# Optimization experiments

Measured on AMD Instinct MI355X. Metric: run time of the kernel, lower is better.

Reference implementation:

```python
import jax, jax.numpy as jnp
import numpy as np

H = 32        # num_attention_heads
KVH = 8       # num_key_value_heads
D = 64        # attention_head_size
WIN = 256     # attention_window_size (left/right)
ROPE_BASE = 10000.0


def setup_inputs() -> dict:
    key = jax.random.key(0)
    k1, k2, k3 = jax.random.split(key, 3)
    B, S = 2, 2048
    return {
        "query_states": jax.random.normal(k1, (B, S, H * D), dtype=jnp.float32),
        "key_states": jax.random.normal(k2, (B, S, KVH * D), dtype=jnp.float32),
        "value_states": jax.random.normal(k3, (B, S, KVH * D), dtype=jnp.float32),
    }


def _rope_cos_sin(seq_len, dtype):
    inv_freq = 1.0 / (ROPE_BASE ** (jnp.arange(0, D, 2, dtype=jnp.float32) / D))  # [D/2]
    pos = jnp.arange(seq_len, dtype=jnp.float32)
    freqs = pos[:, None] * inv_freq[None, :]          # [S, D/2]
    emb = jnp.concatenate([freqs, freqs], axis=-1)    # [S, D]
    return jnp.cos(emb).astype(dtype), jnp.sin(emb).astype(dtype)


def _rotate_half(x):
    x1, x2 = x[..., : D // 2], x[..., D // 2 :]
    return jnp.concatenate([-x2, x1], axis=-1)


def reference(query_states, key_states, value_states):
    B, S, _ = query_states.shape
    n_rep = H // KVH

    q = query_states.reshape(B, S, H, D).transpose(0, 2, 1, 3)        # [B,H,S,D]
    k = key_states.reshape(B, S, KVH, D).transpose(0, 2, 1, 3)        # [B,KVH,S,D]
    v = value_states.reshape(B, S, KVH, D).transpose(0, 2, 1, 3)

    # repeat_kv: [B,KVH,S,D] -> [B,H,S,D]
    k = jnp.repeat(k, n_rep, axis=1)
    v = jnp.repeat(v, n_rep, axis=1)

    cos, sin = _rope_cos_sin(S, q.dtype)   # [S,D]
    cos = cos[None, None]                  # [1,1,S,D]
    sin = sin[None, None]
    q = q * cos + _rotate_half(q) * sin
    k = k * cos + _rotate_half(k) * sin

    scale = 1.0 / jnp.sqrt(jnp.asarray(D, dtype=q.dtype))
    scores = jnp.einsum("bhqd,bhkd->bhqk", q, k) * scale              # [B,H,S,S]

    i = jnp.arange(S)[:, None]
    j = jnp.arange(S)[None, :]
    allowed = (j >= i - WIN) & (j <= i)                               # [S,S]
    scores = jnp.where(allowed[None, None], scores, jnp.finfo(scores.dtype).min)

    probs = jax.nn.softmax(scores, axis=-1)
    out = jnp.einsum("bhqk,bhkd->bhqd", probs, v)                     # [B,H,S,D]
    return out.transpose(0, 2, 1, 3).reshape(B, S, H * D)
```

## Files before the change

### kernel.cpp

```cpp
#include <hip/hip_runtime.h>
#include <math.h>

#define NH   32
#define NKVH 8
#define HD   64
#define WIN  256
#define BB   2
#define SS   2048

typedef short short8 __attribute__((ext_vector_type(8)));
typedef float f32x4  __attribute__((ext_vector_type(4)));

__device__ __forceinline__ ushort f2bf(float x) {
    union { float f; unsigned u; } v; v.f = x;
    unsigned u = v.u + 0x7FFF + ((v.u >> 16) & 1);
    return (ushort)(u >> 16);
}

__device__ __forceinline__ int cvtpk_bf16(float lo, float hi) {
    int r;
    asm("v_cvt_pk_bf16_f32 %0, %1, %2" : "=v"(r) : "v"(lo), "v"(hi));
    return r;
}

__device__ __forceinline__ int swz(int L) { return L ^ (((L >> 7) & 7) << 4); }

__device__ __forceinline__ void stage16(const void* g, void* l) {
    __builtin_amdgcn_global_load_lds(
        (const __attribute__((address_space(1))) unsigned int*)g,
        (__attribute__((address_space(3))) unsigned int*)l, 16, 0, 0);
}

__global__ __launch_bounds__(256) void prep_kv(const float* __restrict__ K,
                                               const float* __restrict__ V,
                                               ushort* __restrict__ Kr,
                                               ushort* __restrict__ Vt) {
    __shared__ __align__(16) ushort ldsK[2048];
    __shared__ __align__(16) ushort ldsV[2048];
    const int bidx = blockIdx.x;
    const int sblk = bidx & 63;
    const int s0   = sblk * 32;
    const int kvh  = (bidx >> 6) & 7;
    const int b    = bidx >> 9;
    const int tid  = threadIdx.x;

    {
        const int key = tid >> 3, dg = tid & 7;
        const int s   = s0 + key;
        const float* krow = K + (size_t)(b * SS + s) * (NKVH * HD) + kvh * HD + dg * 8;
        float x[8];
        *(float4*)(x)     = *(const float4*)(krow);
        *(float4*)(x + 4) = *(const float4*)(krow + 4);
        float inv = __powf(10000.f, -(float)((dg & 3) * 8) * (1.f / 32.f));
        const float ratio = 0.74989420933f;
        ushort out[8];
#pragma unroll
        for (int j = 0; j < 8; ++j) {
            float partner = __shfl(x[j], (tid & 63) ^ 4, 64);
            float sn, cs;
            __sincosf((float)s * inv, &sn, &cs);
            out[j] = f2bf(x[j] * cs + ((dg < 4) ? -partner : partner) * sn);
            inv *= ratio;
        }
        *(short8*)((char*)ldsK + swz(key * 128 + dg * 16)) = *(short8*)out;
    }
    {
        const int kp = tid & 15, dq = tid >> 4;
        const float* v0 = V + (size_t)(b * SS + s0 + 2 * kp) * (NKVH * HD) + kvh * HD + dq * 4;
        float4 a = *(const float4*)v0;
        float4 c = *(const float4*)(v0 + NKVH * HD);
#pragma unroll
        for (int j = 0; j < 4; ++j) {
            int d = dq * 4 + j;
            unsigned w = (unsigned)f2bf(((const float*)&a)[j])
                       | ((unsigned)f2bf(((const float*)&c)[j]) << 16);
            *(unsigned*)((char*)ldsV + swz(d * 64 + kp * 4)) = w;
        }
    }
    __syncthreads();
    char* kc = (char*)(Kr + (size_t)(b * NKVH + kvh) * SS * HD) + (size_t)sblk * 4096;
    char* vc = (char*)(Vt + (size_t)(b * NKVH + kvh) * HD * SS) + (size_t)sblk * 4096;
    *(short8*)(kc + tid * 16) = *(short8*)((char*)ldsK + tid * 16);
    *(short8*)(vc + tid * 16) = *(short8*)((char*)ldsV + tid * 16);
}

__global__ __launch_bounds__(256, 4) void attn_mfma(const float* __restrict__ Q,
                                                    const ushort* __restrict__ Kr,
                                                    const ushort* __restrict__ Vt,
                                                    float* __restrict__ O) {
    __shared__ __align__(16) ushort ldsK[2][2048];
    __shared__ __align__(16) ushort ldsV[2][2048];
    const int wv = threadIdx.x >> 6, lane = threadIdx.x & 63;
    const int lo16 = lane & 15, quad = lane >> 4;
    const int bidx = (blockIdx.x & 7) * 128 + (blockIdx.x >> 3);
    const int qblk = bidx & 63;
    const int kvh  = (bidx >> 6) & 7;
    const int b    = bidx >> 9;
    const int h    = kvh * 4 + wv;
    const int q0   = qblk * 32;

    float invf[8];
#pragma unroll
    for (int j = 0; j < 8; ++j)
        invf[j] = __powf(10000.f, -(float)(quad * 8 + j) * (1.f / 32.f));

    short8 aq[2][2];
#pragma unroll
    for (int t = 0; t < 2; ++t) {
        int qi = q0 + t * 16 + lo16;
        const float* qrow = Q + (size_t)(b * SS + qi) * (NH * HD) + h * HD;
        float lo[8], hi[8];
        *(float4*)(lo)     = *(const float4*)(qrow + quad * 8);
        *(float4*)(lo + 4) = *(const float4*)(qrow + quad * 8 + 4);
        *(float4*)(hi)     = *(const float4*)(qrow + 32 + quad * 8);
        *(float4*)(hi + 4) = *(const float4*)(qrow + 32 + quad * 8 + 4);
#pragma unroll
        for (int j = 0; j < 8; ++j) {
            float sn, cs;
            __sincosf((float)qi * invf[j], &sn, &cs);
            aq[t][0][j] = (short)f2bf((lo[j] * cs - hi[j] * sn) * 0.125f);
            aq[t][1][j] = (short)f2bf((hi[j] * cs + lo[j] * sn) * 0.125f);
        }
    }

    const char* kbase = (const char*)(Kr + (size_t)(b * NKVH + kvh) * SS * HD);
    const char* vbase = (const char*)(Vt + (size_t)(b * NKVH + kvh) * HD * SS);

    f32x4 acc[2][4];
#pragma unroll
    for (int t = 0; t < 2; ++t)
#pragma unroll
        for (int i = 0; i < 4; ++i) acc[t][i] = (f32x4){0.f, 0.f, 0.f, 0.f};
    float psum[2] = {0.f, 0.f};

    const int idxAB = (lo16 + ((quad & 1) << 5)) << 2;
    const int idxCD = idxAB + 64;
    const bool hiq  = quad >= 2;

    int klo = q0 - WIN; if (klo < 0) klo = 0;
    const int c0  = klo >> 5;
    const int cnt = (q0 >> 5) - c0 + 1;

    {
        const char* kc = kbase + (size_t)c0 * 4096 + wv * 1024 + lane * 16;
        const char* vc = vbase + (size_t)c0 * 4096 + wv * 1024 + lane * 16;
        stage16(kc, (char*)&ldsK[0][0] + wv * 1024);
        stage16(vc, (char*)&ldsV[0][0] + wv * 1024);
    }
    __syncthreads();

    int nb = 0;
    for (int it = 0; it < cnt; ++it, nb ^= 1) {
        const int kb = klo + it * 32;
        if (it + 1 < cnt) {
            const char* kc = kbase + (size_t)(c0 + it + 1) * 4096 + wv * 1024 + lane * 16;
            const char* vc = vbase + (size_t)(c0 + it + 1) * 4096 + wv * 1024 + lane * 16;
            stage16(kc, (char*)&ldsK[nb ^ 1][0] + wv * 1024);
            stage16(vc, (char*)&ldsV[nb ^ 1][0] + wv * 1024);
        }

        const char* kl = (const char*)&ldsK[nb][0];
        short8 k0 = *(const short8*)(kl + swz(lo16 * 128 + quad * 16));
        short8 k1 = *(const short8*)(kl + swz(lo16 * 128 + 64 + quad * 16));
        short8 k2 = *(const short8*)(kl + swz((lo16 + 16) * 128 + quad * 16));
        short8 k3 = *(const short8*)(kl + swz((lo16 + 16) * 128 + 64 + quad * 16));

        const f32x4 z = {0.f, 0.f, 0.f, 0.f};
        __builtin_amdgcn_s_setprio(1);
        f32x4 s00 = __builtin_amdgcn_mfma_f32_16x16x32_bf16(k0, aq[0][0], z,   0, 0, 0);
        s00       = __builtin_amdgcn_mfma_f32_16x16x32_bf16(k1, aq[0][1], s00, 0, 0, 0);
        f32x4 s01 = __builtin_amdgcn_mfma_f32_16x16x32_bf16(k2, aq[0][0], z,   0, 0, 0);
        s01       = __builtin_amdgcn_mfma_f32_16x16x32_bf16(k3, aq[0][1], s01, 0, 0, 0);
        f32x4 s10 = __builtin_amdgcn_mfma_f32_16x16x32_bf16(k0, aq[1][0], z,   0, 0, 0);
        s10       = __builtin_amdgcn_mfma_f32_16x16x32_bf16(k1, aq[1][1], s10, 0, 0, 0);
        f32x4 s11 = __builtin_amdgcn_mfma_f32_16x16x32_bf16(k2, aq[1][0], z,   0, 0, 0);
        s11       = __builtin_amdgcn_mfma_f32_16x16x32_bf16(k3, aq[1][1], s11, 0, 0, 0);
        __builtin_amdgcn_s_setprio(0);

        short8 ap[2];
#pragma unroll
        for (int t = 0; t < 2; ++t) {
            const f32x4 sa = t ? s10 : s00;
            const f32x4 sb = t ? s11 : s01;
            const int qtmin = q0 + t * 16;
            const int myq   = qtmin + lo16;
            float p[8];
            if ((kb + 31 > qtmin) || (kb < qtmin + 15 - WIN)) {
#pragma unroll
                for (int r = 0; r < 4; ++r) {
                    int key0 = kb + quad * 4 + r;
                    int key1 = key0 + 16;
                    p[r]     = (key0 <= myq && key0 >= myq - WIN) ? __expf(sa[r]) : 0.f;
                    p[4 + r] = (key1 <= myq && key1 >= myq - WIN) ? __expf(sb[r]) : 0.f;
                }
            } else {
#pragma unroll
                for (int r = 0; r < 4; ++r) { p[r] = __expf(sa[r]); p[4 + r] = __expf(sb[r]); }
            }
            psum[t] += ((p[0] + p[1]) + (p[2] + p[3])) + ((p[4] + p[5]) + (p[6] + p[7]));

            int w0 = cvtpk_bf16(p[0], p[1]);
            int w1 = cvtpk_bf16(p[2], p[3]);
            int w2 = cvtpk_bf16(p[4], p[5]);
            int w3 = cvtpk_bf16(p[6], p[7]);
            int a0 = __builtin_amdgcn_ds_bpermute(idxAB, w0);
            int a2 = __builtin_amdgcn_ds_bpermute(idxAB, w2);
            int b1 = __builtin_amdgcn_ds_bpermute(idxAB, w1);
            int b3 = __builtin_amdgcn_ds_bpermute(idxAB, w3);
            int cc0 = __builtin_amdgcn_ds_bpermute(idxCD, w0);
            int cc2 = __builtin_amdgcn_ds_bpermute(idxCD, w2);
            int d1 = __builtin_amdgcn_ds_bpermute(idxCD, w1);
            int d3 = __builtin_amdgcn_ds_bpermute(idxCD, w3);
            union { int i[4]; short8 s; } u;
            u.i[0] = hiq ? a2  : a0;
            u.i[1] = hiq ? b3  : b1;
            u.i[2] = hiq ? cc2 : cc0;
            u.i[3] = hiq ? d3  : d1;
            ap[t] = u.s;
        }

        const char* vl = (const char*)&ldsV[nb][0];
        short8 vf[4];
#pragma unroll
        for (int i = 0; i < 4; ++i)
            vf[i] = *(const short8*)(vl + swz((i * 16 + lo16) * 64 + quad * 16));

        __builtin_amdgcn_s_setprio(1);
#pragma unroll
        for (int i = 0; i < 4; ++i)
            acc[0][i] = __builtin_amdgcn_mfma_f32_16x16x32_bf16(ap[0], vf[i], acc[0][i], 0, 0, 0);
#pragma unroll
        for (int i = 0; i < 4; ++i)
            acc[1][i] = __builtin_amdgcn_mfma_f32_16x16x32_bf16(ap[1], vf[i], acc[1][i], 0, 0, 0);
        __builtin_amdgcn_s_setprio(0);

        __syncthreads();
    }

#pragma unroll
    for (int t = 0; t < 2; ++t) {
        float ps = psum[t];
        ps += __shfl_xor(ps, 16, 64);
        ps += __shfl_xor(ps, 32, 64);
#pragma unroll
        for (int r = 0; r < 4; ++r) {
            float invr = 1.f / __shfl(ps, quad * 4 + r, 16);
            int qr = q0 + t * 16 + quad * 4 + r;
            size_t orow = ((size_t)(b * SS + qr) * NH + h) * HD;
            O[orow + 0 * 16 + lo16] = acc[t][0][r] * invr;
            O[orow + 1 * 16 + lo16] = acc[t][1][r] * invr;
            O[orow + 2 * 16 + lo16] = acc[t][2][r] * invr;
            O[orow + 3 * 16 + lo16] = acc[t][3][r] * invr;
        }
    }
}

__device__ __forceinline__ float wave_sum(float x) {
#pragma unroll
    for (int off = 32; off > 0; off >>= 1) x += __shfl_xor(x, off, 64);
    return x;
}

__global__ __launch_bounds__(256) void attn_scalar(const float* __restrict__ Q,
                                                   const float* __restrict__ K,
                                                   const float* __restrict__ V,
                                                   float* __restrict__ O) {
    int wave = blockIdx.x * 4 + (threadIdx.x >> 6);
    int lane = threadIdx.x & 63;
    int q  = wave % SS;
    int bh = wave / SS;
    int h  = bh % NH;
    int b  = bh / NH;
    int kvh = h >> 2;

    float inv = __powf(10000.f, -(float)(lane & 31) * (1.f / 32.f));
    float sn, cs;
    __sincosf((float)q * inv, &sn, &cs);

    float qv = Q[(size_t)(b * SS + q) * (NH * HD) + h * HD + lane];
    float qpart = __shfl(qv, lane ^ 32, 64);
    float qrot = (qv * cs + ((lane < 32) ? -qpart : qpart) * sn) * 0.125f;

    const float* vbase = V + (size_t)b * SS * (NKVH * HD) + kvh * HD;
    float m = -1e30f, l = 0.f, acc = 0.f;
    int k0 = q - WIN; if (k0 < 0) k0 = 0;
    for (int k = k0; k <= q; ++k) {
        float kraw = K[(size_t)(b * SS + k) * (NKVH * HD) + kvh * HD + lane];
        float kpart = __shfl(kraw, lane ^ 32, 64);
        float ksn, kcs;
        __sincosf((float)k * inv, &ksn, &kcs);
        float kv = kraw * kcs + ((lane < 32) ? -kpart : kpart) * ksn;
        float vv = vbase[(size_t)k * (NKVH * HD) + lane];
        float score = wave_sum(qrot * kv);
        float mnew  = fmaxf(m, score);
        float alpha = __expf(m - mnew);
        float p     = __expf(score - mnew);
        l   = l * alpha + p;
        acc = acc * alpha + p * vv;
        m   = mnew;
    }
    O[(((size_t)(b * SS + q) * NH) + h) * HD + lane] = acc / l;
}

extern "C" void kernel_launch(void* const* d_in, const int* in_sizes, int n_in,
                              void* d_out, int out_size, void* d_ws, size_t ws_size,
                              hipStream_t stream) {
    const float* Q = (const float*)d_in[0];
    const float* K = (const float*)d_in[1];
    const float* V = (const float*)d_in[2];
    float* O = (float*)d_out;

    size_t kv_elems = (size_t)BB * NKVH * SS * HD;
    size_t need = 2 * kv_elems * sizeof(ushort);

    if (ws_size >= need) {
        ushort* Kr = (ushort*)d_ws;
        ushort* Vt = Kr + kv_elems;
        prep_kv<<<BB * NKVH * (SS / 32), 256, 0, stream>>>(K, V, Kr, Vt);
        attn_mfma<<<BB * NKVH * (SS / 32), 256, 0, stream>>>(Q, Kr, Vt, O);
    } else {
        attn_scalar<<<(BB * NH * SS) / 4, 256, 0, stream>>>(Q, K, V, O);
    }
}
```

Measured before the change: 115.4 us.

## Stage K/V in pairs of chunks with vmcnt-based async prefetch

```diff
diff --git a/kernel.cpp b/kernel.cpp
--- a/kernel.cpp
+++ b/kernel.cpp
@@ -88,8 +88,8 @@
                                                     const ushort* __restrict__ Kr,
                                                     const ushort* __restrict__ Vt,
                                                     float* __restrict__ O) {
-    __shared__ __align__(16) ushort ldsK[2][2048];
-    __shared__ __align__(16) ushort ldsV[2][2048];
+    __shared__ __align__(16) ushort ldsK[2][2][2048];
+    __shared__ __align__(16) ushort ldsV[2][2][2048];
     const int wv = threadIdx.x >> 6, lane = threadIdx.x & 63;
     const int lo16 = lane & 15, quad = lane >> 4;
     const int bidx = (blockIdx.x & 7) * 128 + (blockIdx.x >> 3);
@@ -140,26 +140,23 @@
     int klo = q0 - WIN; if (klo < 0) klo = 0;
     const int c0  = klo >> 5;
     const int cnt = (q0 >> 5) - c0 + 1;
-
-    {
-        const char* kc = kbase + (size_t)c0 * 4096 + wv * 1024 + lane * 16;
-        const char* vc = vbase + (size_t)c0 * 4096 + wv * 1024 + lane * 16;
-        stage16(kc, (char*)&ldsK[0][0] + wv * 1024);
-        stage16(vc, (char*)&ldsV[0][0] + wv * 1024);
-    }
-    __syncthreads();
-
-    int nb = 0;
-    for (int it = 0; it < cnt; ++it, nb ^= 1) {
-        const int kb = klo + it * 32;
-        if (it + 1 < cnt) {
-            const char* kc = kbase + (size_t)(c0 + it + 1) * 4096 + wv * 1024 + lane * 16;
-            const char* vc = vbase + (size_t)(c0 + it + 1) * 4096 + wv * 1024 + lane * 16;
-            stage16(kc, (char*)&ldsK[nb ^ 1][0] + wv * 1024);
-            stage16(vc, (char*)&ldsV[nb ^ 1][0] + wv * 1024);
-        }
-
-        const char* kl = (const char*)&ldsK[nb][0];
+    const int npairs = (cnt + 1) >> 1;
+
+    auto stagepair = [&](int pidx, int buf) {
+        int ca = c0 + 2 * pidx, cb = ca + 1;
+        if (ca > SS / 32 - 1) ca = SS / 32 - 1;
+        if (cb > SS / 32 - 1) cb = SS / 32 - 1;
+        stage16(kbase + (size_t)ca * 4096 + wv * 1024 + lane * 16,
+                (char*)&ldsK[buf][0][0] + wv * 1024);
+        stage16(vbase + (size_t)ca * 4096 + wv * 1024 + lane * 16,
+                (char*)&ldsV[buf][0][0] + wv * 1024);
+        stage16(kbase + (size_t)cb * 4096 + wv * 1024 + lane * 16,
+                (char*)&ldsK[buf][1][0] + wv * 1024);
+        stage16(vbase + (size_t)cb * 4096 + wv * 1024 + lane * 16,
+                (char*)&ldsV[buf][1][0] + wv * 1024);
+    };
+
+    auto compute = [&](int kb, const char* kl, const char* vl) {
         short8 k0 = *(const short8*)(kl + swz(lo16 * 128 + quad * 16));
         short8 k1 = *(const short8*)(kl + swz(lo16 * 128 + 64 + quad * 16));
         short8 k2 = *(const short8*)(kl + swz((lo16 + 16) * 128 + quad * 16));
@@ -219,7 +216,6 @@
             ap[t] = u.s;
         }
 
-        const char* vl = (const char*)&ldsV[nb][0];
         short8 vf[4];
 #pragma unroll
         for (int i = 0; i < 4; ++i)
@@ -233,8 +229,21 @@
         for (int i = 0; i < 4; ++i)
             acc[1][i] = __builtin_amdgcn_mfma_f32_16x16x32_bf16(ap[1], vf[i], acc[1][i], 0, 0, 0);
         __builtin_amdgcn_s_setprio(0);
-
-        __syncthreads();
+    };
+
+    stagepair(0, 0);
+
+    int nb = 0;
+    for (int p = 0; p < npairs; ++p, nb ^= 1) {
+        stagepair(p + 1, nb ^ 1);
+        asm volatile("s_waitcnt vmcnt(4)" ::: "memory");
+        __builtin_amdgcn_s_barrier();
+        __builtin_amdgcn_sched_barrier(0);
+        compute(klo + 2 * p * 32, (const char*)&ldsK[nb][0][0], (const char*)&ldsV[nb][0][0]);
+        if (2 * p + 1 < cnt)
+            compute(klo + (2 * p + 1) * 32, (const char*)&ldsK[nb][1][0], (const char*)&ldsV[nb][1][0]);
+        __builtin_amdgcn_sched_barrier(0);
+        __builtin_amdgcn_s_barrier();
     }
 
 #pragma unroll
```

Measured after the change: 114.6 us. About the same (-0.7%).
